# Optimization experiments

Measured on AMD Instinct MI355X. Metric: run time of the kernel, lower is better.

The kernel has to match this reference:

```python
import jax, jax.numpy as jnp
import numpy as np


def _conv1x1(W, x):
    # W: (out_c, in_c) from a 1x1 Conv2d (bias=False); x: (b, in_c, h, w)
    return jnp.einsum('oc,bchw->bohw', W, x)


def setup_inputs() -> dict:
    key = jax.random.key(0)
    ks = jax.random.split(key, 7)
    b, c, h, w = 4, 256, 64, 64
    inter = c // 2
    out_c = 256
    s = 0.02
    return {
        'A': jax.random.normal(ks[0], (b, c, h, w), dtype=jnp.float32),
        'B': jax.random.normal(ks[1], (b, c, h, w), dtype=jnp.float32),
        'W_phi': jax.random.normal(ks[2], (inter, c), dtype=jnp.float32) * s,
        'W_theta': jax.random.normal(ks[3], (inter, c), dtype=jnp.float32) * s,
        'W_g': jax.random.normal(ks[4], (inter, 2 * c), dtype=jnp.float32) * s,
        'W_AB': jax.random.normal(ks[5], (out_c, 2 * c), dtype=jnp.float32) * s,
        'W_mask': jax.random.normal(ks[6], (out_c, inter), dtype=jnp.float32) * s,
    }


def reference(A, B, W_phi, W_theta, W_g, W_AB, W_mask):
    b, c, h, w = A.shape
    inter = c // 2
    AB = jnp.concatenate([A, B], axis=1)  # (b, 2c, h, w)
    # NOTE: original torch code views (b, c/2, h*w) as (b, c, h*w/2) -> seq len N = h*w/2
    x_phi = _conv1x1(W_phi, A).reshape(b, c, -1)                       # (b, c, N)
    x_theta = _conv1x1(W_theta, B).reshape(b, c, -1).transpose(0, 2, 1)  # (b, N, c)
    x_g = _conv1x1(W_g, AB).reshape(b, c, -1).transpose(0, 2, 1)       # (b, N, c)
    scores = jnp.einsum('bnc,bcm->bnm', x_theta, x_phi)                # (b, N, N)
    attn = jax.nn.softmax(scores, axis=1)  # softmax over dim=1 as in torch code
    y = jnp.einsum('bnm,bmc->bnc', attn, x_g)                          # (b, N, c)
    y = y.transpose(0, 2, 1).reshape(b, inter, h, w)
    out = _conv1x1(W_mask, y) + _conv1x1(W_AB, AB)
    return out
```

## Files before the change

kernel.cpp:

```cpp
#include <hip/hip_runtime.h>
#include <hip/hip_bf16.h>

#define B_    4
#define C_    256
#define HW    4096
#define N_    2048
#define BSTR  524288

typedef unsigned short u16;
using f32x4 = __attribute__((ext_vector_type(4))) float;
using u32x4 = __attribute__((ext_vector_type(4))) unsigned int;

__device__ __forceinline__ float bf2f(u16 u) {
    return __uint_as_float(((unsigned)u) << 16);
}
__device__ __forceinline__ u16 f2bf(float f) {
    unsigned x = __float_as_uint(f);
    x += 0x7fff + ((x >> 16) & 1);
    return (u16)(x >> 16);
}

__device__ __forceinline__ void mfma_bf16(f32x4& acc, u32x4 a, u32x4 b) {
    asm volatile("v_mfma_f32_16x16x32_bf16 %0, %1, %2, %0"
                 : "+v"(acc) : "v"(a), "v"(b));
}
__device__ __forceinline__ void mfma_bf16_vsrc(f32x4& acc, u32x4 a, u32x4 b) {
    asm volatile("s_nop 1\n\tv_mfma_f32_16x16x32_bf16 %0, %1, %2, %0"
                 : "+v"(acc) : "v"(a), "v"(b));
}
__device__ __forceinline__ void mfma_fence(f32x4& x) {
    asm volatile("s_nop 7\n\ts_nop 7" : "+v"(x));
}

__global__ __launch_bounds__(256) void prep_w(
    const float* __restrict__ Wphi, const float* __restrict__ Wtheta,
    const float* __restrict__ Wg, const float* __restrict__ Wab,
    u16* __restrict__ Wt)
{
    const int row = blockIdx.x;
    const int t   = threadIdx.x;
    #pragma unroll
    for (int i = 0; i < 2; ++i) {
        const int col = i * 256 + t;
        float v;
        if (row < 128)      v = (col < 256)  ? Wphi[row * 256 + col] : 0.f;
        else if (row < 256) v = (col >= 256) ? Wtheta[(row - 128) * 256 + (col - 256)] : 0.f;
        else if (row < 384) v = Wg[(row - 256) * 512 + col];
        else                v = Wab[(row - 384) * 512 + col];
        Wt[row * 512 + col] = f2bf(v);
    }
}

__global__ __launch_bounds__(256) void prep_abt(
    const float* __restrict__ A, const float* __restrict__ Bx,
    u16* __restrict__ ABt)
{
    __shared__ u16 L[64][528];
    const int t = threadIdx.x, pb = blockIdx.x, b = blockIdx.y;
    const int p0 = pb * 64;
    const int pl = t & 63, cg = t >> 6;
    const float* Ab = A  + (size_t)b * C_ * HW;
    const float* Bb = Bx + (size_t)b * C_ * HW;

    for (int i = 0; i < 64; ++i) {
        const int c = cg + i * 4;
        L[pl][c]       = f2bf(Ab[c * HW + p0 + pl]);
        L[pl][256 + c] = f2bf(Bb[c * HW + p0 + pl]);
    }
    __syncthreads();
    u16* dst = ABt + ((size_t)b * 4096 + p0) * 512;
    #pragma unroll
    for (int i = 0; i < 16; ++i) {
        const int idx = i * 256 + t;
        const int row = idx >> 6, ch = idx & 63;
        *(uint4*)&dst[row * 512 + ch * 8] = *(const uint4*)&L[row][ch * 8];
    }
}

__global__ __launch_bounds__(256) void conv_gemm(
    const u16* __restrict__ Wt, const u16* __restrict__ ABt,
    u16* __restrict__ phit, u16* __restrict__ thetat,
    u16* __restrict__ g, float* __restrict__ out)
{
    __shared__ __align__(16) u16 shW[64 * 128];
    __shared__ __align__(16) u16 shAB[64 * 128];
    const int t = threadIdx.x, pb = blockIdx.x, nb = blockIdx.y, b = blockIdx.z;
    const int lane = t & 63, w = t >> 6, lo = lane & 15, hi = lane >> 4;
    const u16* Wb = Wt + nb * 64 * 512;
    const u16* Ab = ABt + ((size_t)b * 4096 + pb * 64) * 512;

    f32x4 acc[4];
    #pragma unroll
    for (int ot = 0; ot < 4; ++ot) acc[ot] = (f32x4){0.f, 0.f, 0.f, 0.f};

    for (int ks = 0; ks < 4; ++ks) {
        __syncthreads();
        #pragma unroll
        for (int i = 0; i < 4; ++i) {
            const int q = i * 256 + t;
            const int row = q >> 4, c16 = (q & 15) * 8;
            const int sw = (row & 7) << 3;
            *(uint4*)&shW[row * 128 + (c16 ^ sw)]  = *(const uint4*)&Wb[row * 512 + ks * 128 + c16];
            *(uint4*)&shAB[row * 128 + (c16 ^ sw)] = *(const uint4*)&Ab[row * 512 + ks * 128 + c16];
        }
        __syncthreads();
        u32x4 bfr[4];
        {
            const int row = w * 16 + lo, sw = (row & 7) << 3;
            #pragma unroll
            for (int kf = 0; kf < 4; ++kf)
                bfr[kf] = *(const u32x4*)&shAB[row * 128 + ((kf * 32 + hi * 8) ^ sw)];
        }
        #pragma unroll
        for (int ot = 0; ot < 4; ++ot) {
            const int row = ot * 16 + lo, sw = (row & 7) << 3;
            #pragma unroll
            for (int kf = 0; kf < 4; ++kf) {
                const u32x4 a = *(const u32x4*)&shW[row * 128 + ((kf * 32 + hi * 8) ^ sw)];
                mfma_bf16(acc[ot], a, bfr[kf]);
            }
        }
    }

    const int p_global = pb * 64 + w * 16 + lo;
    const int m = p_global & 2047, h = p_global >> 11;
    #pragma unroll
    for (int ot = 0; ot < 4; ++ot) {
        mfma_fence(acc[ot]);
        const int ob = nb * 64 + ot * 16 + hi * 4;
        if (nb < 2) {
            ushort4 v;
            v.x = f2bf(acc[ot][0]); v.y = f2bf(acc[ot][1]);
            v.z = f2bf(acc[ot][2]); v.w = f2bf(acc[ot][3]);
            *(ushort4*)&phit[(size_t)b * BSTR + m * 256 + h * 128 + ob] = v;
        } else if (nb < 4) {
            ushort4 v;
            v.x = f2bf(acc[ot][0]); v.y = f2bf(acc[ot][1]);
            v.z = f2bf(acc[ot][2]); v.w = f2bf(acc[ot][3]);
            *(ushort4*)&thetat[(size_t)b * BSTR + m * 256 + h * 128 + (ob - 128)] = v;
        } else if (nb < 6) {
            #pragma unroll
            for (int q = 0; q < 4; ++q)
                g[(size_t)b * BSTR + (ob - 256 + q) * HW + p_global] = f2bf(acc[ot][q]);
        } else {
            #pragma unroll
            for (int q = 0; q < 4; ++q)
                out[(size_t)b * C_ * HW + (size_t)(ob - 384 + q) * HW + p_global] = acc[ot][q];
        }
    }
}

__global__ __launch_bounds__(256) void passA_mfma(
    const u16* __restrict__ phit, const u16* __restrict__ thetat,
    float* __restrict__ rs)
{
    __shared__ __align__(16) u16 shP[64 * 256];
    __shared__ __align__(16) u16 shT[64 * 256];
    const int t = threadIdx.x, b = blockIdx.z, nq = blockIdx.y, mb = blockIdx.x;
    const u16* Pb = phit   + b * BSTR + mb * 64 * 256;
    const u16* Tb = thetat + b * BSTR + nq * 512 * 256;

    #pragma unroll
    for (int i = 0; i < 8; ++i) {
        const int q = i * 256 + t;
        const int row = q >> 5, c16 = (q & 31) * 8;
        const uint4 v = *(const uint4*)&Pb[row * 256 + c16];
        *(uint4*)&shP[row * 256 + (c16 ^ ((row & 7) << 3))] = v;
    }
    __syncthreads();

    const int lane = t & 63, w = t >> 6, lo = lane & 15, hi = lane >> 4;
    u32x4 afr[8];
    {
        const int row = w * 16 + lo;
        #pragma unroll
        for (int kb = 0; kb < 8; ++kb)
            afr[kb] = *(const u32x4*)&shP[row * 256 + ((kb * 32 + hi * 8) ^ ((row & 7) << 3))];
    }

    float rsacc[4] = {0.f, 0.f, 0.f, 0.f};
    for (int nt = 0; nt < 8; ++nt) {
        __syncthreads();
        #pragma unroll
        for (int i = 0; i < 8; ++i) {
            const int q = i * 256 + t;
            const int row = q >> 5, c16 = (q & 31) * 8;
            const uint4 v = *(const uint4*)&Tb[(nt * 64 + row) * 256 + c16];
            *(uint4*)&shT[row * 256 + (c16 ^ ((row & 7) << 3))] = v;
        }
        __syncthreads();
        #pragma unroll
        for (int ns = 0; ns < 4; ++ns) {
            f32x4 acc = {0.f, 0.f, 0.f, 0.f};
            const int row = ns * 16 + lo;
            #pragma unroll
            for (int kb = 0; kb < 8; ++kb) {
                const u32x4 bfr = *(const u32x4*)&shT[row * 256 + ((kb * 32 + hi * 8) ^ ((row & 7) << 3))];
                mfma_bf16(acc, afr[kb], bfr);
            }
            mfma_fence(acc);
            rsacc[0] += __expf(acc.x); rsacc[1] += __expf(acc.y);
            rsacc[2] += __expf(acc.z); rsacc[3] += __expf(acc.w);
        }
    }
    #pragma unroll
    for (int q = 0; q < 4; ++q) {
        float v = rsacc[q];
        v += __shfl_xor(v, 1); v += __shfl_xor(v, 2);
        v += __shfl_xor(v, 4); v += __shfl_xor(v, 8);
        rsacc[q] = v;
    }
    if (lo == 0) {
        const int m = mb * 64 + w * 16 + hi * 4;
        float* dst = rs + (nq * 4 + b) * N_ + m;
        dst[0] = rsacc[0]; dst[1] = rsacc[1]; dst[2] = rsacc[2]; dst[3] = rsacc[3];
    }
}

__global__ __launch_bounds__(256) void g_scale(
    const float* __restrict__ rs, u16* __restrict__ g)
{
    const int t  = threadIdx.x;
    const int mt = blockIdx.x;
    const int cg = blockIdx.y;
    const int b  = blockIdx.z;
    const int m  = mt * 256 + t;
    const float* rp = rs + b * N_ + m;
    const float inv = 1.0f / (rp[0] + rp[8192] + rp[16384] + rp[24576]);
    u16* gb = g + (size_t)b * BSTR + cg * 8 * N_ + m;
    #pragma unroll
    for (int j = 0; j < 8; ++j)
        gb[j * N_] = f2bf(bf2f(gb[j * N_]) * inv);
}

__global__ __launch_bounds__(256) void passB_mfma(
    const u16* __restrict__ phit, const u16* __restrict__ thetat,
    const u16* __restrict__ g, u16* __restrict__ ytp)
{
    __shared__ __align__(16) u16 shBuf[2][17408];
    const int t = threadIdx.x, b = blockIdx.z, mq = blockIdx.y, nb = blockIdx.x;
    const u16* Tb = thetat + b * BSTR + nb * 64 * 256;
    const u16* Pb = phit   + b * BSTR + mq * 512 * 256;
    const u16* Gb = g      + b * BSTR + mq * 512;
    const int lane = t & 63, w = t >> 6, lo = lane & 15, hi = lane >> 4;

    u16* shT = &shBuf[0][0];
    #pragma unroll
    for (int i = 0; i < 8; ++i) {
        const int q = i * 256 + t;
        const int row = q >> 5, c16 = (q & 31) * 8;
        const uint4 v = *(const uint4*)&Tb[row * 256 + c16];
        *(uint4*)&shT[row * 256 + (c16 ^ ((row & 7) << 3))] = v;
    }
    __syncthreads();
    u32x4 bfr[8];
    {
        const int row = w * 16 + lo;
        #pragma unroll
        for (int kb = 0; kb < 8; ++kb)
            bfr[kb] = *(const u32x4*)&shT[row * 256 + ((kb * 32 + hi * 8) ^ ((row & 7) << 3))];
    }
    __syncthreads();

    f32x4 accY[16];
    #pragma unroll
    for (int ct = 0; ct < 16; ++ct) accY[ct] = (f32x4){0.f, 0.f, 0.f, 0.f};

    uint4 vp[4], vg[4];
    #pragma unroll
    for (int i = 0; i < 4; ++i) {
        const int q = i * 256 + t;
        vp[i] = *(const uint4*)&Pb[(q >> 5) * 256 + (q & 31) * 8];
    }
    #pragma unroll
    for (int qd = 0; qd < 4; ++qd)
        vg[qd] = *(const uint4*)&Gb[(size_t)t * N_ + qd * 8];

    for (int mt = 0; mt < 16; ++mt) {
        u16* shPm = &shBuf[mt & 1][0];
        u16* shG  = &shBuf[mt & 1][8192];

        #pragma unroll
        for (int i = 0; i < 4; ++i) {
            const int q = i * 256 + t;
            const int row = q >> 5, c16 = (q & 31) * 8;
            *(uint4*)&shPm[row * 256 + (c16 ^ ((row & 7) << 3))] = vp[i];
        }
        {
            u16* gr = &shG[t * 36];
            *(uint2*)&gr[0]  = make_uint2(vg[0].x, vg[0].y);
            *(uint2*)&gr[4]  = make_uint2(vg[0].z, vg[0].w);
            *(uint2*)&gr[8]  = make_uint2(vg[1].x, vg[1].y);
            *(uint2*)&gr[12] = make_uint2(vg[1].z, vg[1].w);
            *(uint2*)&gr[16] = make_uint2(vg[2].x, vg[2].y);
            *(uint2*)&gr[20] = make_uint2(vg[2].z, vg[2].w);
            *(uint2*)&gr[24] = make_uint2(vg[3].x, vg[3].y);
            *(uint2*)&gr[28] = make_uint2(vg[3].z, vg[3].w);
        }
        const int mtn = (mt < 15) ? mt + 1 : 15;
        #pragma unroll
        for (int i = 0; i < 4; ++i) {
            const int q = i * 256 + t;
            vp[i] = *(const uint4*)&Pb[(mtn * 32 + (q >> 5)) * 256 + (q & 31) * 8];
        }
        #pragma unroll
        for (int qd = 0; qd < 4; ++qd)
            vg[qd] = *(const uint4*)&Gb[(size_t)t * N_ + mtn * 32 + qd * 8];

        __syncthreads();

        __builtin_amdgcn_s_setprio(1);
        f32x4 s0 = {0.f, 0.f, 0.f, 0.f}, s1 = {0.f, 0.f, 0.f, 0.f};
        {
            const int row = lo;
            #pragma unroll
            for (int kb = 0; kb < 8; ++kb) {
                const u32x4 a = *(const u32x4*)&shPm[row * 256 + ((kb * 32 + hi * 8) ^ ((row & 7) << 3))];
                mfma_bf16(s0, a, bfr[kb]);
            }
        }
        {
            const int row = 16 + lo;
            #pragma unroll
            for (int kb = 0; kb < 8; ++kb) {
                const u32x4 a = *(const u32x4*)&shPm[row * 256 + ((kb * 32 + hi * 8) ^ ((row & 7) << 3))];
                mfma_bf16(s1, a, bfr[kb]);
            }
        }
        __builtin_amdgcn_s_setprio(0);
        mfma_fence(s0); mfma_fence(s1);

        float p0[4], p1[4];
        #pragma unroll
        for (int q = 0; q < 4; ++q) {
            p0[q] = __expf(s0[q]);
            p1[q] = __expf(s1[q]);
        }
        u32x4 pf;
        pf[0] = (unsigned)f2bf(p0[0]) | ((unsigned)f2bf(p0[1]) << 16);
        pf[1] = (unsigned)f2bf(p0[2]) | ((unsigned)f2bf(p0[3]) << 16);
        pf[2] = (unsigned)f2bf(p1[0]) | ((unsigned)f2bf(p1[1]) << 16);
        pf[3] = (unsigned)f2bf(p1[2]) | ((unsigned)f2bf(p1[3]) << 16);

        __builtin_amdgcn_s_setprio(1);
        #pragma unroll
        for (int ct = 0; ct < 16; ++ct) {
            const int row = ct * 16 + lo;
            const uint2 a0 = *(const uint2*)&shG[row * 36 + hi * 4];
            const uint2 a1 = *(const uint2*)&shG[row * 36 + 16 + hi * 4];
            u32x4 gf; gf[0] = a0.x; gf[1] = a0.y; gf[2] = a1.x; gf[3] = a1.y;
            if (ct == 0) mfma_bf16_vsrc(accY[ct], gf, pf);
            else         mfma_bf16(accY[ct], gf, pf);
        }
        __builtin_amdgcn_s_setprio(0);
    }

    u16* Yb = ytp + ((size_t)mq * B_ + b) * BSTR;
    const int col = nb * 64 + w * 16 + lo;
    #pragma unroll
    for (int ct = 0; ct < 16; ++ct) {
        mfma_fence(accY[ct]);
        const int crow = ct * 16 + hi * 4;
        #pragma unroll
        for (int q = 0; q < 4; ++q)
            Yb[(crow + q) * N_ + col] = f2bf(accY[ct][q]);
    }
}

__global__ __launch_bounds__(256) void mask_add_kernel(
    const u16* __restrict__ ytp, const float* __restrict__ Wm,
    float* __restrict__ out)
{
    const int p  = blockIdx.x * 256 + threadIdx.x;
    const int og = blockIdx.y;
    const int b  = blockIdx.z;
    const u16* Y0 = ytp + (size_t)(0 * B_ + b) * BSTR;
    const u16* Y1 = ytp + (size_t)(1 * B_ + b) * BSTR;
    const u16* Y2 = ytp + (size_t)(2 * B_ + b) * BSTR;
    const u16* Y3 = ytp + (size_t)(3 * B_ + b) * BSTR;

    float acc[8] = {};
    for (int k = 0; k < 128; ++k) {
        const float y = bf2f(Y0[k * HW + p]) + bf2f(Y1[k * HW + p])
                      + bf2f(Y2[k * HW + p]) + bf2f(Y3[k * HW + p]);
        #pragma unroll
        for (int j = 0; j < 8; ++j)
            acc[j] = fmaf(Wm[(og * 8 + j) * 128 + k], y, acc[j]);
    }
    float* ob = out + (size_t)b * C_ * HW;
    #pragma unroll
    for (int j = 0; j < 8; ++j)
        ob[(og * 8 + j) * HW + p] += acc[j];
}

extern "C" void kernel_launch(void* const* d_in, const int* in_sizes, int n_in,
                              void* d_out, int out_size, void* d_ws, size_t ws_size,
                              hipStream_t stream)
{
    const float* A      = (const float*)d_in[0];
    const float* Bx     = (const float*)d_in[1];
    const float* Wphi   = (const float*)d_in[2];
    const float* Wtheta = (const float*)d_in[3];
    const float* Wg     = (const float*)d_in[4];
    const float* Wab    = (const float*)d_in[5];
    const float* Wmask  = (const float*)d_in[6];
    float* out = (float*)d_out;

    u16*   ABt    = (u16*)d_ws;
    u16*   ytp    = ABt;
    u16*   Wt     = ABt + 8388608;
    u16*   phit   = Wt + 327680;
    u16*   thetat = phit + 2097152;
    u16*   g      = thetat + 2097152;
    float* rs     = (float*)(g + 2097152);

    prep_w<<<dim3(640), 256, 0, stream>>>(Wphi, Wtheta, Wg, Wab, Wt);

    prep_abt<<<dim3(64, 4), 256, 0, stream>>>(A, Bx, ABt);

    conv_gemm<<<dim3(64, 10, 4), 256, 0, stream>>>(
        Wt, ABt, phit, thetat, g, out);

    passA_mfma<<<dim3(32, 4, 4), 256, 0, stream>>>(phit, thetat, rs);

    g_scale<<<dim3(8, 32, 4), 256, 0, stream>>>(rs, g);

    passB_mfma<<<dim3(32, 4, 4), 256, 0, stream>>>(phit, thetat, g, ytp);

    mask_add_kernel<<<dim3(16, 32, 4), 256, 0, stream>>>(ytp, Wmask, out);
}
```

Before: 256.6 us.

## Use MFMA builtins, vectorize prep loads, stage Y output through LDS

Replaces the inline-asm MFMA wrappers and their manual s_nop fences with the compiler builtin, so the compiler can schedule around MFMA latency instead of padding with fixed nops. The setprio hints are removed. The prep_abt transpose now reads float4 vectors instead of scalar loads. The attention kernel's Y output is staged through shared memory so each thread writes contiguous 128-byte rows rather than scattered 2-byte stores. The risks are that compiler scheduling may be worse than the hand-placed code, and that the shBuf reuse needs enough space (256 rows x 72).

Measured after the change: 259.2 us. No clear change (+1.0%).

```diff
diff --git a/kernel.cpp b/kernel.cpp
--- a/kernel.cpp
+++ b/kernel.cpp
@@ -8,8 +8,8 @@
 #define BSTR  524288
 
 typedef unsigned short u16;
-using f32x4 = __attribute__((ext_vector_type(4))) float;
-using u32x4 = __attribute__((ext_vector_type(4))) unsigned int;
+using f32x4  = __attribute__((ext_vector_type(4))) float;
+using bf16x8 = __attribute__((ext_vector_type(8))) short;
 
 __device__ __forceinline__ float bf2f(u16 u) {
     return __uint_as_float(((unsigned)u) << 16);
@@ -20,16 +20,11 @@
     return (u16)(x >> 16);
 }
 
-__device__ __forceinline__ void mfma_bf16(f32x4& acc, u32x4 a, u32x4 b) {
-    asm volatile("v_mfma_f32_16x16x32_bf16 %0, %1, %2, %0"
-                 : "+v"(acc) : "v"(a), "v"(b));
-}
-__device__ __forceinline__ void mfma_bf16_vsrc(f32x4& acc, u32x4 a, u32x4 b) {
-    asm volatile("s_nop 1\n\tv_mfma_f32_16x16x32_bf16 %0, %1, %2, %0"
-                 : "+v"(acc) : "v"(a), "v"(b));
-}
-__device__ __forceinline__ void mfma_fence(f32x4& x) {
-    asm volatile("s_nop 7\n\ts_nop 7" : "+v"(x));
+__device__ __forceinline__ f32x4 mfma(bf16x8 a, bf16x8 b, f32x4 c) {
+    return __builtin_amdgcn_mfma_f32_16x16x32_bf16(a, b, c, 0, 0, 0);
+}
+__device__ __forceinline__ bf16x8 ld_frag(const u16* p) {
+    return *(const bf16x8*)p;
 }
 
 __global__ __launch_bounds__(256) void prep_w(
@@ -58,14 +53,20 @@
     __shared__ u16 L[64][528];
     const int t = threadIdx.x, pb = blockIdx.x, b = blockIdx.y;
     const int p0 = pb * 64;
-    const int pl = t & 63, cg = t >> 6;
+    const int tq = t & 15;
+    const int cr = t >> 4;
     const float* Ab = A  + (size_t)b * C_ * HW;
     const float* Bb = Bx + (size_t)b * C_ * HW;
 
-    for (int i = 0; i < 64; ++i) {
-        const int c = cg + i * 4;
-        L[pl][c]       = f2bf(Ab[c * HW + p0 + pl]);
-        L[pl][256 + c] = f2bf(Bb[c * HW + p0 + pl]);
+    #pragma unroll 4
+    for (int i = 0; i < 16; ++i) {
+        const int c = i * 16 + cr;
+        const float4 va = *(const float4*)&Ab[(size_t)c * HW + p0 + tq * 4];
+        const float4 vb = *(const float4*)&Bb[(size_t)c * HW + p0 + tq * 4];
+        L[tq * 4 + 0][c] = f2bf(va.x); L[tq * 4 + 1][c] = f2bf(va.y);
+        L[tq * 4 + 2][c] = f2bf(va.z); L[tq * 4 + 3][c] = f2bf(va.w);
+        L[tq * 4 + 0][256 + c] = f2bf(vb.x); L[tq * 4 + 1][256 + c] = f2bf(vb.y);
+        L[tq * 4 + 2][256 + c] = f2bf(vb.z); L[tq * 4 + 3][256 + c] = f2bf(vb.w);
     }
     __syncthreads();
     u16* dst = ABt + ((size_t)b * 4096 + p0) * 512;
@@ -104,21 +105,20 @@
             *(uint4*)&shAB[row * 128 + (c16 ^ sw)] = *(const uint4*)&Ab[row * 512 + ks * 128 + c16];
         }
         __syncthreads();
-        u32x4 bfr[4];
+        bf16x8 bfr[4];
         {
             const int row = w * 16 + lo, sw = (row & 7) << 3;
             #pragma unroll
             for (int kf = 0; kf < 4; ++kf)
-                bfr[kf] = *(const u32x4*)&shAB[row * 128 + ((kf * 32 + hi * 8) ^ sw)];
+                bfr[kf] = ld_frag(&shAB[row * 128 + ((kf * 32 + hi * 8) ^ sw)]);
         }
         #pragma unroll
         for (int ot = 0; ot < 4; ++ot) {
             const int row = ot * 16 + lo, sw = (row & 7) << 3;
             #pragma unroll
-            for (int kf = 0; kf < 4; ++kf) {
-                const u32x4 a = *(const u32x4*)&shW[row * 128 + ((kf * 32 + hi * 8) ^ sw)];
-                mfma_bf16(acc[ot], a, bfr[kf]);
-            }
+            for (int kf = 0; kf < 4; ++kf)
+                acc[ot] = mfma(ld_frag(&shW[row * 128 + ((kf * 32 + hi * 8) ^ sw)]),
+                               bfr[kf], acc[ot]);
         }
     }
 
@@ -126,7 +126,6 @@
     const int m = p_global & 2047, h = p_global >> 11;
     #pragma unroll
     for (int ot = 0; ot < 4; ++ot) {
-        mfma_fence(acc[ot]);
         const int ob = nb * 64 + ot * 16 + hi * 4;
         if (nb < 2) {
             ushort4 v;
@@ -170,12 +169,12 @@
     __syncthreads();
 
     const int lane = t & 63, w = t >> 6, lo = lane & 15, hi = lane >> 4;
-    u32x4 afr[8];
+    bf16x8 afr[8];
     {
         const int row = w * 16 + lo;
         #pragma unroll
         for (int kb = 0; kb < 8; ++kb)
-            afr[kb] = *(const u32x4*)&shP[row * 256 + ((kb * 32 + hi * 8) ^ ((row & 7) << 3))];
+            afr[kb] = ld_frag(&shP[row * 256 + ((kb * 32 + hi * 8) ^ ((row & 7) << 3))]);
     }
 
     float rsacc[4] = {0.f, 0.f, 0.f, 0.f};
@@ -194,11 +193,10 @@
             f32x4 acc = {0.f, 0.f, 0.f, 0.f};
             const int row = ns * 16 + lo;
             #pragma unroll
-            for (int kb = 0; kb < 8; ++kb) {
-                const u32x4 bfr = *(const u32x4*)&shT[row * 256 + ((kb * 32 + hi * 8) ^ ((row & 7) << 3))];
-                mfma_bf16(acc, afr[kb], bfr);
-            }
-            mfma_fence(acc);
+            for (int kb = 0; kb < 8; ++kb)
+                acc = mfma(afr[kb],
+                           ld_frag(&shT[row * 256 + ((kb * 32 + hi * 8) ^ ((row & 7) << 3))]),
+                           acc);
             rsacc[0] += __expf(acc.x); rsacc[1] += __expf(acc.y);
             rsacc[2] += __expf(acc.z); rsacc[3] += __expf(acc.w);
         }
@@ -253,12 +251,12 @@
         *(uint4*)&shT[row * 256 + (c16 ^ ((row & 7) << 3))] = v;
     }
     __syncthreads();
-    u32x4 bfr[8];
+    bf16x8 bfr[8];
     {
         const int row = w * 16 + lo;
         #pragma unroll
         for (int kb = 0; kb < 8; ++kb)
-            bfr[kb] = *(const u32x4*)&shT[row * 256 + ((kb * 32 + hi * 8) ^ ((row & 7) << 3))];
+            bfr[kb] = ld_frag(&shT[row * 256 + ((kb * 32 + hi * 8) ^ ((row & 7) << 3))]);
     }
     __syncthreads();
 
@@ -309,61 +307,56 @@
 
         __syncthreads();
 
-        __builtin_amdgcn_s_setprio(1);
         f32x4 s0 = {0.f, 0.f, 0.f, 0.f}, s1 = {0.f, 0.f, 0.f, 0.f};
         {
             const int row = lo;
             #pragma unroll
-            for (int kb = 0; kb < 8; ++kb) {
-                const u32x4 a = *(const u32x4*)&shPm[row * 256 + ((kb * 32 + hi * 8) ^ ((row & 7) << 3))];
-                mfma_bf16(s0, a, bfr[kb]);
-            }
+            for (int kb = 0; kb < 8; ++kb)
+                s0 = mfma(ld_frag(&shPm[row * 256 + ((kb * 32 + hi * 8) ^ ((row & 7) << 3))]),
+                          bfr[kb], s0);
         }
         {
             const int row = 16 + lo;
             #pragma unroll
-            for (int kb = 0; kb < 8; ++kb) {
-                const u32x4 a = *(const u32x4*)&shPm[row * 256 + ((kb * 32 + hi * 8) ^ ((row & 7) << 3))];
-                mfma_bf16(s1, a, bfr[kb]);
-            }
-        }
-        __builtin_amdgcn_s_setprio(0);
-        mfma_fence(s0); mfma_fence(s1);
-
-        float p0[4], p1[4];
-        #pragma unroll
-        for (int q = 0; q < 4; ++q) {
-            p0[q] = __expf(s0[q]);
-            p1[q] = __expf(s1[q]);
-        }
-        u32x4 pf;
-        pf[0] = (unsigned)f2bf(p0[0]) | ((unsigned)f2bf(p0[1]) << 16);
-        pf[1] = (unsigned)f2bf(p0[2]) | ((unsigned)f2bf(p0[3]) << 16);
-        pf[2] = (unsigned)f2bf(p1[0]) | ((unsigned)f2bf(p1[1]) << 16);
-        pf[3] = (unsigned)f2bf(p1[2]) | ((unsigned)f2bf(p1[3]) << 16);
-
-        __builtin_amdgcn_s_setprio(1);
+            for (int kb = 0; kb < 8; ++kb)
+                s1 = mfma(ld_frag(&shPm[row * 256 + ((kb * 32 + hi * 8) ^ ((row & 7) << 3))]),
+                          bfr[kb], s1);
+        }
+
+        union { unsigned u[4]; bf16x8 h; } pfu;
+        pfu.u[0] = (unsigned)f2bf(__expf(s0[0])) | ((unsigned)f2bf(__expf(s0[1])) << 16);
+        pfu.u[1] = (unsigned)f2bf(__expf(s0[2])) | ((unsigned)f2bf(__expf(s0[3])) << 16);
+        pfu.u[2] = (unsigned)f2bf(__expf(s1[0])) | ((unsigned)f2bf(__expf(s1[1])) << 16);
+        pfu.u[3] = (unsigned)f2bf(__expf(s1[2])) | ((unsigned)f2bf(__expf(s1[3])) << 16);
+        const bf16x8 pf = pfu.h;
+
         #pragma unroll
         for (int ct = 0; ct < 16; ++ct) {
             const int row = ct * 16 + lo;
-            const uint2 a0 = *(const uint2*)&shG[row * 36 + hi * 4];
-            const uint2 a1 = *(const uint2*)&shG[row * 36 + 16 + hi * 4];
-            u32x4 gf; gf[0] = a0.x; gf[1] = a0.y; gf[2] = a1.x; gf[3] = a1.y;
-            if (ct == 0) mfma_bf16_vsrc(accY[ct], gf, pf);
-            else         mfma_bf16(accY[ct], gf, pf);
-        }
-        __builtin_amdgcn_s_setprio(0);
-    }
-
-    u16* Yb = ytp + ((size_t)mq * B_ + b) * BSTR;
-    const int col = nb * 64 + w * 16 + lo;
+            union { uint2 v[2]; bf16x8 h; } gfu;
+            gfu.v[0] = *(const uint2*)&shG[row * 36 + hi * 4];
+            gfu.v[1] = *(const uint2*)&shG[row * 36 + 16 + hi * 4];
+            accY[ct] = mfma(gfu.h, pf, accY[ct]);
+        }
+    }
+
+    __syncthreads();
+    u16* shY = &shBuf[0][0];
     #pragma unroll
     for (int ct = 0; ct < 16; ++ct) {
-        mfma_fence(accY[ct]);
         const int crow = ct * 16 + hi * 4;
         #pragma unroll
         for (int q = 0; q < 4; ++q)
-            Yb[(crow + q) * N_ + col] = f2bf(accY[ct][q]);
+            shY[(crow + q) * 72 + w * 16 + lo] = f2bf(accY[ct][q]);
+    }
+    __syncthreads();
+    u16* Yb = ytp + ((size_t)mq * B_ + b) * BSTR + nb * 64;
+    {
+        const u16* src = &shY[t * 72];
+        u16* dstg = &Yb[(size_t)t * N_];
+        #pragma unroll
+        for (int k = 0; k < 8; ++k)
+            *(uint4*)&dstg[k * 8] = *(const uint4*)&src[k * 8];
     }
 }
 
```
